# Performance work log

Hardware: AMD Instinct MI355X
Metric: run time of the kernel (lower is better)

Reference implementation:

```python
import jax, jax.numpy as jnp
import numpy as np

# ---- fixed opt values from source ----
B = 10
IN_C = 3
IN_HW = 64
OUT_VIEW_N = 8
OUT_H = 128
OUT_W = 128
RENDER_DEPTH = 1.0
LATENT = 512
KHOM2DTO3D = np.array([[64, 0, 0, 32], [0, -64, 0, 32], [0, 0, -1, 0], [0, 0, 0, 1]], dtype=np.float32)


def quat_to_rotmat(q):
    # q: [V,4] (w,x,y,z)
    w, x, y, z = q[:, 0], q[:, 1], q[:, 2], q[:, 3]
    R = jnp.stack([
        1 - 2 * (y * y + z * z), 2 * (x * y - w * z), 2 * (x * z + w * y),
        2 * (x * y + w * z), 1 - 2 * (x * x + z * z), 2 * (y * z - w * x),
        2 * (x * z - w * y), 2 * (y * z + w * x), 1 - 2 * (x * x + y * y),
    ], axis=-1).reshape(-1, 3, 3)
    return R


def conv(x, w, b, stride=2):
    y = jax.lax.conv_general_dilated(x, w, (stride, stride), 'SAME',
                                     dimension_numbers=('NCHW', 'OIHW', 'NCHW'))
    return y + b[None, :, None, None]


def deconv(x, w, b):
    # stride-2 transposed conv, kernel 4, SAME-like (doubles spatial size)
    y = jax.lax.conv_transpose(x, w, (2, 2), 'SAME',
                               dimension_numbers=('NCHW', 'OIHW', 'NCHW'),
                               transpose_kernel=True)
    return y + b[None, :, None, None]


def setup_inputs() -> dict:
    key = jax.random.key(0)
    ks = jax.random.split(key, 24)
    s = 0.05
    d = {}
    d['x'] = jax.random.normal(ks[0], (B, IN_C, IN_HW, IN_HW), dtype=jnp.float32)
    # encoder convs: 3->96->128->192->256 (stride 2 each, 64->4), then fc -> latent
    enc_ch = [IN_C, 96, 128, 192, 256]
    for i in range(4):
        d[f'ew{i}'] = jax.random.normal(ks[1 + i], (enc_ch[i + 1], enc_ch[i], 3, 3)) * s
        d[f'eb{i}'] = jnp.zeros((enc_ch[i + 1],), jnp.float32)
    d['efw'] = jax.random.normal(ks[5], (256 * 4 * 4, LATENT)) * s
    d['efb'] = jnp.zeros((LATENT,), jnp.float32)
    # decoder: fc latent -> 256*4*4, deconvs 256->192->128->96->64->48 (4->128)
    d['dfw'] = jax.random.normal(ks[6], (LATENT, 256 * 4 * 4)) * s
    d['dfb'] = jnp.zeros((256 * 4 * 4,), jnp.float32)
    dec_ch = [256, 192, 128, 96, 64, 48]
    for i in range(5):
        d[f'dw{i}'] = jax.random.normal(ks[7 + i], (dec_ch[i], dec_ch[i + 1], 4, 4)) * s
        d[f'db{i}'] = jnp.zeros((dec_ch[i + 1],), jnp.float32)
    # heads: 1x1 conv -> XYZ (V*3) and mask logits (V)
    d['xyzw'] = jax.random.normal(ks[12], (OUT_VIEW_N * 3, dec_ch[-1], 1, 1)) * s
    d['xyzb'] = jnp.zeros((OUT_VIEW_N * 3,), jnp.float32)
    d['maskw'] = jax.random.normal(ks[13], (OUT_VIEW_N, dec_ch[-1], 1, 1)) * s
    d['maskb'] = jnp.zeros((OUT_VIEW_N,), jnp.float32)
    # fuseTrans: fixed per-view quaternions (normalized)
    q = jax.random.normal(ks[14], (OUT_VIEW_N, 4))
    d['fuseTrans'] = q / jnp.linalg.norm(q, axis=-1, keepdims=True)
    return d


def _forward(x, ew0, eb0, ew1, eb1, ew2, eb2, ew3, eb3, efw, efb,
             dfw, dfb, dw0, db0, dw1, db1, dw2, db2, dw3, db3, dw4, db4,
             xyzw, xyzb, maskw, maskb, fuseTrans):
    relu = jax.nn.relu
    # encoder
    h = relu(conv(x, ew0, eb0))
    h = relu(conv(h, ew1, eb1))
    h = relu(conv(h, ew2, eb2))
    h = relu(conv(h, ew3, eb3))  # [B,256,4,4]
    latent = relu(h.reshape(B, -1) @ efw + efb)
    # decoder
    h = relu(latent @ dfw + dfb).reshape(B, 256, 4, 4)
    h = relu(deconv(h, dw0, db0))
    h = relu(deconv(h, dw1, db1))
    h = relu(deconv(h, dw2, db2))
    h = relu(deconv(h, dw3, db3))
    h = relu(deconv(h, dw4, db4))  # [B,48,128,128]
    XYZ = conv(h, xyzw, xyzb, stride=1)        # [B,V*3,H,W]
    maskLogit = conv(h, maskw, maskb, stride=1)  # [B,V,H,W]
    # ---- fuse3D ----
    V, H, W = OUT_VIEW_N, OUT_H, OUT_W
    XYZ = XYZ.reshape(B, V, 3, H, W)
    X = XYZ[:, :, 0].reshape(B, V, -1)
    Y = XYZ[:, :, 1].reshape(B, V, -1)
    Z = XYZ[:, :, 2].reshape(B, V, -1) + RENDER_DEPTH  # predicted depth offset
    ones = jnp.ones_like(X)
    XYZhom = jnp.stack([X, Y, Z, ones], axis=2)  # [B,V,4,HW]
    # inverse-project 2D grid coords + depth to 3D camera coords
    Kinv = jnp.asarray(np.linalg.inv(KHOM2DTO3D))  # [4,4]
    XYZcam = jnp.einsum('ij,bvjn->bvin', Kinv, XYZhom)[:, :, :3]  # [B,V,3,HW]
    # rotate each view into canonical frame via fuseTrans quaternions
    R = quat_to_rotmat(fuseTrans)  # [V,3,3] cam->world
    RT = jnp.swapaxes(R, 1, 2)
    XYZid = jnp.einsum('vij,bvjn->bvin', RT, XYZcam)  # [B,V,3,HW]
    XYZid = jnp.transpose(XYZid, (0, 2, 1, 3)).reshape(B, 3, V * H * W)
    ML = maskLogit.reshape(B, 1, V * H * W)
    return XYZid, ML


def reference(x, ew0, eb0, ew1, eb1, ew2, eb2, ew3, eb3, efw, efb,
              dfw, dfb, dw0, db0, dw1, db1, dw2, db2, dw3, db3, dw4, db4,
              xyzw, xyzb, maskw, maskb, fuseTrans):
    return _forward(x, ew0, eb0, ew1, eb1, ew2, eb2, ew3, eb3, efw, efb,
                    dfw, dfb, dw0, db0, dw1, db1, dw2, db2, dw3, db3, dw4, db4,
                    xyzw, xyzb, maskw, maskb, fuseTrans)
```

## Files before the change

### kernel.cpp

```cpp
#include <hip/hip_runtime.h>

#define CDIV(a,b) (((a)+(b)-1)/(b))

typedef short short8v __attribute__((ext_vector_type(8)));
typedef float f32x4 __attribute__((ext_vector_type(4)));

__device__ __forceinline__ ushort f2bf(float v) {
    uint u = __float_as_uint(v);
    return (ushort)((u + 0x7FFF + ((u >> 16) & 1)) >> 16);
}

__global__ __launch_bounds__(256) void conv3x3_c3(const float* __restrict__ in,
    const float* __restrict__ w, const float* __restrict__ bias, float* __restrict__ out)
{
    int idx = blockIdx.x * 256 + threadIdx.x;
    int ox = idx & 31; int t = idx >> 5;
    int oy = t & 31;   t >>= 5;
    int co = t % 96;   int b = t / 96;
    float acc = bias[co];
    const float* wp  = w + co * 27;
    const float* ipb = in + (size_t)b * 3 * 64 * 64;
    #pragma unroll
    for (int ci = 0; ci < 3; ++ci) {
        #pragma unroll
        for (int ky = 0; ky < 3; ++ky) {
            int iy = 2 * oy + ky;
            #pragma unroll
            for (int kx = 0; kx < 3; ++kx) {
                int ix = 2 * ox + kx;
                if (iy < 64 && ix < 64)
                    acc = fmaf(wp[ci * 9 + ky * 3 + kx], ipb[(ci * 64 + iy) * 64 + ix], acc);
            }
        }
    }
    out[idx] = fmaxf(acc, 0.f);
}

template<int CIN,int COUT,int HIN,int WIN,int SPLITS,int CK,int CO_R>
__global__ __launch_bounds__(256) void conv_splitk_big(const float* __restrict__ in,
    const float* __restrict__ w, float* __restrict__ partial)
{
    constexpr int HOUT = HIN/2, WOUT = WIN/2;
    constexpr int SP = HOUT * WOUT;
    static_assert(SP == 256, "one output px per thread");
    constexpr int HP = HIN + 1, WP = WIN + 2;
    constexpr int CSL = CIN / SPLITS;
    constexpr int NCH = CSL / CK;
    static_assert(CSL % CK == 0, "CK must divide ci slice");
    constexpr int SELEM = CK * HP * WP;
    constexpr int NLD = (SELEM + 255) / 256;
    __shared__ float sb[SELEM];

    const int b = blockIdx.y, s = blockIdx.z;
    const int co_base = blockIdx.x * CO_R;
    const int oy = threadIdx.x >> 4, ox = threadIdx.x & 15;
    const int ci00 = s * CSL;
    const float* inb = in + (size_t)b * CIN * HIN * WIN;

    float rg[NLD];
    auto load_chunk = [&](int ci0) {
        #pragma unroll
        for (int j = 0; j < NLD; ++j) {
            int i = threadIdx.x + j * 256;
            float v = 0.f;
            if (i < SELEM) {
                int c = i % WP; int r = (i / WP) % HP; int cl = i / (WP * HP);
                if (r < HIN && c < WIN) v = inb[((size_t)(ci0 + cl) * HIN + r) * WIN + c];
            }
            rg[j] = v;
        }
    };
    load_chunk(ci00);

    float acc[CO_R] = {};
    for (int ch = 0; ch < NCH; ++ch) {
        #pragma unroll
        for (int j = 0; j < NLD; ++j) {
            int i = threadIdx.x + j * 256;
            if (i < SELEM) sb[i] = rg[j];
        }
        __syncthreads();
        if (ch + 1 < NCH) load_chunk(ci00 + (ch + 1) * CK);

        #pragma unroll
        for (int cl = 0; cl < CK; ++cl) {
            const float* sp = &sb[(cl * HP + 2 * oy) * WP + 2 * ox];
            float x[3][3];
            #pragma unroll
            for (int dy = 0; dy < 3; ++dy) {
                float2 f = *(const float2*)&sp[dy * WP];
                x[dy][0] = f.x; x[dy][1] = f.y; x[dy][2] = sp[dy * WP + 2];
            }
            int ci = ci00 + ch * CK + cl;
            const float* wp = w + ((size_t)co_base * CIN + ci) * 9;
            #pragma unroll
            for (int r = 0; r < CO_R; ++r) {
                const float* wr = wp + (size_t)r * CIN * 9;
                #pragma unroll
                for (int dy = 0; dy < 3; ++dy)
                    #pragma unroll
                    for (int dx = 0; dx < 3; ++dx)
                        acc[r] = fmaf(wr[dy * 3 + dx], x[dy][dx], acc[r]);
            }
        }
        __syncthreads();
    }
    #pragma unroll
    for (int r = 0; r < CO_R; ++r)
        partial[(((size_t)s * 10 + b) * COUT + co_base + r) * SP + threadIdx.x] = acc[r];
}

template<int CIN,int COUT,int HIN,int WIN,int CK,int CO_R,int COS>
__global__ __launch_bounds__(256) void conv_small_splitk(const float* __restrict__ in,
    const float* __restrict__ w, float* __restrict__ partial)
{
    constexpr int HOUT = HIN/2, WOUT = WIN/2;
    constexpr int SP = HOUT * WOUT;
    static_assert(SP * COS == 256, "block covers SP x COS");
    constexpr int HP = HIN + 1, WP = WIN + 2;
    __shared__ float sb[CK * HP * WP];
    const int b = blockIdx.y;
    const int s = blockIdx.z;
    const int sp_i = threadIdx.x % SP;
    const int slot = threadIdx.x / SP;
    const int co_base = (blockIdx.x * COS + slot) * CO_R;
    const int oy = sp_i / WOUT, ox = sp_i % WOUT;
    const int ci0 = s * CK;
    const float* inb = in + (size_t)b * CIN * HIN * WIN;

    for (int i = threadIdx.x; i < CK * HP * WP; i += 256) {
        int c = i % WP; int r = (i / WP) % HP; int cl = i / (WP * HP);
        float v = 0.f;
        if (r < HIN && c < WIN) v = inb[((size_t)(ci0 + cl) * HIN + r) * WIN + c];
        sb[i] = v;
    }
    __syncthreads();

    float acc[CO_R] = {};
    #pragma unroll
    for (int cl = 0; cl < CK; ++cl) {
        const float* sp = &sb[(cl * HP + 2 * oy) * WP + 2 * ox];
        float x[3][3];
        #pragma unroll
        for (int dy = 0; dy < 3; ++dy) {
            float2 f = *(const float2*)&sp[dy * WP];
            x[dy][0] = f.x; x[dy][1] = f.y; x[dy][2] = sp[dy * WP + 2];
        }
        const float* wp = w + ((size_t)co_base * CIN + (ci0 + cl)) * 9;
        #pragma unroll
        for (int r = 0; r < CO_R; ++r) {
            const float* wr = wp + (size_t)r * CIN * 9;
            #pragma unroll
            for (int dy = 0; dy < 3; ++dy)
                #pragma unroll
                for (int dx = 0; dx < 3; ++dx)
                    acc[r] = fmaf(wr[dy * 3 + dx], x[dy][dx], acc[r]);
        }
    }
    #pragma unroll
    for (int r = 0; r < CO_R; ++r)
        partial[(((size_t)s * 10 + b) * COUT + co_base + r) * SP + sp_i] = acc[r];
}

template<int COUT,int SP,int S>
__global__ void conv_reduce_relu(const float* __restrict__ partial, const float* __restrict__ bias,
                                 float* __restrict__ out, int total)
{
    int i = blockIdx.x * 256 + threadIdx.x;
    if (i >= total) return;
    int sp = i % SP; int co = (i / SP) % COUT; int b = i / (SP * COUT);
    float acc = bias[co];
    #pragma unroll
    for (int s = 0; s < S; ++s) acc += partial[(((size_t)s * 10 + b) * COUT + co) * SP + sp];
    out[i] = fmaxf(acc, 0.f);
}

template<int CIN,int COUT>
__global__ __launch_bounds__(256) void prep_wA_g(const float* __restrict__ w, ushort* __restrict__ Abuf)
{
    constexpr int MFR = COUT / 16, NSL = CIN / 8;
    constexpr int TOTAL = 4 * MFR * NSL * 64 * 8;
    int idx = blockIdx.x * 256 + threadIdx.x;
    if (idx >= TOTAL) return;
    int e = idx & 7; int t2 = idx >> 3;
    int lane = t2 & 63; t2 >>= 6;
    int s = t2 % NSL; t2 /= NSL;
    int m = t2 % MFR; int q = t2 / MFR;
    int co = m * 16 + (lane & 15);
    int k = s * 32 + (lane >> 4) * 8 + e;
    int tap = k / CIN, ci = k % CIN;
    const int widx[4][4] = {{5,7,13,15},{4,6,12,14},{1,3,9,11},{0,2,8,10}};
    float v = w[((size_t)ci * COUT + co) * 16 + widx[q][tap]];
    Abuf[idx] = f2bf(v);
}

template<int CIN,int COUT,int HIN,int QPB,int MS>
__global__ __launch_bounds__(256) void deconv_mfma_g(const float* __restrict__ X,
    const ushort* __restrict__ Abuf, const float* __restrict__ bias, float* __restrict__ out)
{
    constexpr int MFR = COUT / 16, NSL = CIN / 8, STR = CIN + 8;
    constexpr int MPB = MFR / MS;
    constexpr int ZQ = 4 / QPB;
    constexpr int WOUT = 2 * HIN, PLANE = 4 * HIN * HIN;
    __shared__ __align__(16) ushort Xs[100 * STR];
    __shared__ float sbias[COUT];
    const int tid = threadIdx.x;
    constexpr int TW = HIN / 8;
    const int t0 = (blockIdx.x / TW) * 8, u0 = (blockIdx.x % TW) * 8;
    const int b = blockIdx.y;
    const int zq = blockIdx.z % ZQ;
    const int ms = blockIdx.z / ZQ;

    const float* Xb = X + (size_t)b * CIN * HIN * HIN;
    for (int i = tid; i < CIN * 100; i += 256) {
        int ci = i / 100, p = i % 100;
        int r = p / 10, c = p % 10;
        int gt = t0 - 1 + r, gu = u0 - 1 + c;
        float v = 0.f;
        if (gt >= 0 && gt < HIN && gu >= 0 && gu < HIN)
            v = Xb[((size_t)ci * HIN + gt) * HIN + gu];
        Xs[p * STR + ci] = f2bf(v);
    }
    if (tid < COUT) sbias[tid] = bias[tid];
    __syncthreads();

    const int w = tid >> 6, lane = tid & 63;
    const int ncol = lane & 15, kg = lane >> 4;
    const int r_n = 2 * w + (ncol >> 3), c_n = ncol & 7;

    #pragma unroll
    for (int qz = 0; qz < QPB; ++qz) {
        const int q = zq * QPB + qz;
        const int py = q >> 1, px = q & 1;
        int ptap[4];
        #pragma unroll
        for (int tp = 0; tp < 4; ++tp) {
            int dy = py - (tp >> 1);
            int dx = px - (tp & 1);
            ptap[tp] = ((r_n + 1 + dy) * 10 + (c_n + 1 + dx)) * STR;
        }
        #pragma unroll
        for (int mm = 0; mm < MPB; ++mm) {
            const int m = ms * MPB + mm;
            f32x4 acc = {0.f, 0.f, 0.f, 0.f};
            const ushort* ab = Abuf + (((size_t)(q * MFR + m) * NSL) * 64 + lane) * 8;
            #pragma unroll
            for (int s = 0; s < NSL; ++s) {
                short8v a = *(const short8v*)(ab + (size_t)s * 64 * 8);
                int tap = (s * 32) / CIN;
                int ci0 = (s * 32) % CIN + kg * 8;
                short8v bf = *(const short8v*)(&Xs[ptap[tap] + ci0]);
                acc = __builtin_amdgcn_mfma_f32_16x16x32_bf16(a, bf, acc, 0, 0, 0);
            }
            int t = t0 + r_n, u = u0 + c_n;
            size_t base = ((size_t)(b * COUT + m * 16 + kg * 4) * (2 * HIN) + (2 * t + py)) * WOUT + (2 * u + px);
            #pragma unroll
            for (int jj = 0; jj < 4; ++jj) {
                float v = acc[jj] + sbias[m * 16 + kg * 4 + jj];
                out[base + (size_t)jj * PLANE] = fmaxf(v, 0.f);
            }
        }
    }
}

__global__ __launch_bounds__(256) void deconv_mfma_d0(const float* __restrict__ X,
    const ushort* __restrict__ Abuf, const float* __restrict__ bias, float* __restrict__ out)
{
    constexpr int CIN = 256, COUT = 192, MFR = 12, NSL = 32, STR = CIN + 8;
    __shared__ __align__(16) ushort Xs[36 * STR];
    __shared__ float sbias[COUT];
    const int tid = threadIdx.x;
    const int b = blockIdx.y, q = blockIdx.z;

    const float* Xb = X + (size_t)b * CIN * 16;
    for (int i = tid; i < CIN * 36; i += 256) {
        int ci = i / 36, p = i % 36;
        int r = p / 6, c = p % 6;
        int gt = r - 1, gu = c - 1;
        float v = 0.f;
        if (gt >= 0 && gt < 4 && gu >= 0 && gu < 4)
            v = Xb[(ci * 4 + gt) * 4 + gu];
        Xs[p * STR + ci] = f2bf(v);
    }
    if (tid < COUT) sbias[tid] = bias[tid];
    __syncthreads();

    const int w = tid >> 6, lane = tid & 63;
    const int ncol = lane & 15, kg = lane >> 4;
    const int r_n = ncol >> 2, c_n = ncol & 3;
    const int py = q >> 1, px = q & 1;

    int ptap[4];
    #pragma unroll
    for (int tp = 0; tp < 4; ++tp) {
        int dy = py - (tp >> 1);
        int dx = px - (tp & 1);
        ptap[tp] = ((r_n + 1 + dy) * 6 + (c_n + 1 + dx)) * STR;
    }
    #pragma unroll
    for (int j = 0; j < 3; ++j) {
        const int m = w + 4 * j;
        f32x4 acc = {0.f, 0.f, 0.f, 0.f};
        const ushort* ab = Abuf + (((size_t)(q * MFR + m) * NSL) * 64 + lane) * 8;
        #pragma unroll
        for (int s = 0; s < NSL; ++s) {
            short8v a = *(const short8v*)(ab + (size_t)s * 64 * 8);
            int tap = s >> 3, ci0 = (s & 7) * 32 + kg * 8;
            short8v bf = *(const short8v*)(&Xs[ptap[tap] + ci0]);
            acc = __builtin_amdgcn_mfma_f32_16x16x32_bf16(a, bf, acc, 0, 0, 0);
        }
        size_t base = ((size_t)(b * COUT + m * 16 + kg * 4) * 8 + (2 * r_n + py)) * 8 + (2 * c_n + px);
        #pragma unroll
        for (int jj = 0; jj < 4; ++jj) {
            float v = acc[jj] + sbias[m * 16 + kg * 4 + jj];
            out[base + (size_t)jj * 64] = fmaxf(v, 0.f);
        }
    }
}

template<int KC>
__global__ __launch_bounds__(256) void fc_splitk(const float* __restrict__ in,
    const float* __restrict__ W, float* __restrict__ partial, int K, int N)
{
    __shared__ float s_in[10 * KC];
    const int o = blockIdx.x * 256 + threadIdx.x;
    const int k0 = blockIdx.y * KC;
    for (int i = threadIdx.x; i < 10 * KC; i += 256) {
        int b = i / KC, k = i % KC;
        s_in[i] = in[(size_t)b * K + k0 + k];
    }
    __syncthreads();

    float acc[10];
    #pragma unroll
    for (int b = 0; b < 10; ++b) acc[b] = 0.f;
    const float* wp = W + (size_t)k0 * N + o;
    #pragma unroll 4
    for (int k = 0; k < KC; ++k) {
        float wv = wp[(size_t)k * N];
        #pragma unroll
        for (int b = 0; b < 10; ++b) acc[b] = fmaf(wv, s_in[b * KC + k], acc[b]);
    }
    float* pp = partial + ((size_t)blockIdx.y * 10) * N + o;
    #pragma unroll
    for (int b = 0; b < 10; ++b) pp[(size_t)b * N] = acc[b];
}

__global__ void fc_reduce_relu(const float* __restrict__ partial, const float* __restrict__ bias,
                               float* __restrict__ out, int N, int S)
{
    int i = blockIdx.x * 256 + threadIdx.x;
    if (i >= 10 * N) return;
    int o = i % N, b = i / N;
    float acc = bias[o];
    for (int s = 0; s < S; ++s) acc += partial[((size_t)s * 10 + b) * N + o];
    out[(size_t)b * N + o] = fmaxf(acc, 0.f);
}

__global__ __launch_bounds__(256) void final_fused_v2(const float* __restrict__ h,
    const float* __restrict__ xyzw, const float* __restrict__ xyzb,
    const float* __restrict__ maskw, const float* __restrict__ maskb,
    const float* __restrict__ quat, float* __restrict__ out)
{
    const int V = 8, HW = 128 * 128, C = 48, Bn = 10, VHW = V * HW;
    __shared__ float4 sh[48 * 32];
    int b = blockIdx.y, tile = blockIdx.x;
    const float4* hb = (const float4*)h;
    for (int i = threadIdx.x; i < C * 32; i += 256) {
        int ci = i >> 5, p = i & 31;
        sh[i] = hb[(size_t)(b * C + ci) * (HW / 4) + tile * 32 + p];
    }
    __syncthreads();

    int pl = threadIdx.x & 31, v = threadIdx.x >> 5;
    float4 xr = {0,0,0,0}, yr = {0,0,0,0}, zr = {0,0,0,0}, mm = {0,0,0,0};
    const float* wx = xyzw + (size_t)(v * 3 + 0) * C;
    const float* wy = xyzw + (size_t)(v * 3 + 1) * C;
    const float* wz = xyzw + (size_t)(v * 3 + 2) * C;
    const float* wm = maskw + (size_t)v * C;
    for (int ci = 0; ci < C; ++ci) {
        float4 hv = sh[ci * 32 + pl];
        float a;
        a = wx[ci]; xr.x += a*hv.x; xr.y += a*hv.y; xr.z += a*hv.z; xr.w += a*hv.w;
        a = wy[ci]; yr.x += a*hv.x; yr.y += a*hv.y; yr.z += a*hv.z; yr.w += a*hv.w;
        a = wz[ci]; zr.x += a*hv.x; zr.y += a*hv.y; zr.z += a*hv.z; zr.w += a*hv.w;
        a = wm[ci]; mm.x += a*hv.x; mm.y += a*hv.y; mm.z += a*hv.z; mm.w += a*hv.w;
    }
    float bxv = xyzb[v * 3 + 0], byv = xyzb[v * 3 + 1], bzv = xyzb[v * 3 + 2], bmv = maskb[v];

    float qw = quat[v*4+0], qx = quat[v*4+1], qy = quat[v*4+2], qz = quat[v*4+3];
    float R00 = 1.f - 2.f*(qy*qy + qz*qz), R01 = 2.f*(qx*qy - qw*qz), R02 = 2.f*(qx*qz + qw*qy);
    float R10 = 2.f*(qx*qy + qw*qz), R11 = 1.f - 2.f*(qx*qx + qz*qz), R12 = 2.f*(qy*qz - qw*qx);
    float R20 = 2.f*(qx*qz - qw*qy), R21 = 2.f*(qy*qz + qw*qx), R22 = 1.f - 2.f*(qx*qx + qy*qy);

    float4 o0, o1, o2, om;
    float* X = (float*)&xr; float* Y = (float*)&yr; float* Z = (float*)&zr; float* M = (float*)&mm;
    float* O0 = (float*)&o0; float* O1 = (float*)&o1; float* O2 = (float*)&o2; float* OM = (float*)&om;
    #pragma unroll
    for (int j = 0; j < 4; ++j) {
        float camX = (X[j] + bxv) * (1.f / 64.f) - 0.5f;
        float camY = -(Y[j] + byv) * (1.f / 64.f) + 0.5f;
        float camZ = -((Z[j] + bzv) + 1.0f);
        O0[j] = R00 * camX + R10 * camY + R20 * camZ;
        O1[j] = R01 * camX + R11 * camY + R21 * camZ;
        O2[j] = R02 * camX + R12 * camY + R22 * camZ;
        OM[j] = M[j] + bmv;
    }

    size_t o = (size_t)v * HW + tile * 128 + pl * 4;
    float4* op = (float4*)out;
    op[((size_t)(b * 3 + 0) * VHW + o) >> 2] = o0;
    op[((size_t)(b * 3 + 1) * VHW + o) >> 2] = o1;
    op[((size_t)(b * 3 + 2) * VHW + o) >> 2] = o2;
    op[((size_t)Bn * 3 * VHW + (size_t)b * VHW + o) >> 2] = om;
}


extern "C" void kernel_launch(void* const* d_in, const int* in_sizes, int n_in,
                              void* d_out, int out_size, void* d_ws, size_t ws_size,
                              hipStream_t stream)
{
    const float* x    = (const float*)d_in[0];
    const float* ew0  = (const float*)d_in[1];
    const float* eb0  = (const float*)d_in[2];
    const float* ew1  = (const float*)d_in[3];
    const float* eb1  = (const float*)d_in[4];
    const float* ew2  = (const float*)d_in[5];
    const float* eb2  = (const float*)d_in[6];
    const float* ew3  = (const float*)d_in[7];
    const float* eb3  = (const float*)d_in[8];
    const float* efw  = (const float*)d_in[9];
    const float* efb  = (const float*)d_in[10];
    const float* dfw  = (const float*)d_in[11];
    const float* dfb  = (const float*)d_in[12];
    const float* dw0  = (const float*)d_in[13];
    const float* db0  = (const float*)d_in[14];
    const float* dw1  = (const float*)d_in[15];
    const float* db1  = (const float*)d_in[16];
    const float* dw2  = (const float*)d_in[17];
    const float* db2  = (const float*)d_in[18];
    const float* dw3  = (const float*)d_in[19];
    const float* db3  = (const float*)d_in[20];
    const float* dw4  = (const float*)d_in[21];
    const float* db4  = (const float*)d_in[22];
    const float* xyzw = (const float*)d_in[23];
    const float* xyzb = (const float*)d_in[24];
    const float* maskw= (const float*)d_in[25];
    const float* maskb= (const float*)d_in[26];
    const float* quat = (const float*)d_in[27];
    float* out = (float*)d_out;

    float* A   = (float*)d_ws;
    float* Bb  = A + 7864320;
    float* P1  = A;
    float* L   = A + 1120000;
    float* P2  = Bb + 1000000;
    float* H0  = Bb;
    float* PC1 = A + 2000000;
    float* PC2 = A + 2000000;
    float* PC3 = Bb + 500000;
    ushort* Abuf4 = (ushort*)(Bb + 2700000);
    ushort* Abuf3 = (ushort*)(A + 1000000);
    ushort* Abuf2 = (ushort*)(A + 1200000);
    ushort* Abuf1 = (ushort*)(A + 1400000);
    ushort* Abuf0 = (ushort*)(A + 1600000);

    const int TB = 256;

    prep_wA_g< 64, 48><<< 192, 256, 0, stream>>>(dw4, Abuf4);
    prep_wA_g< 96, 64><<< 384, 256, 0, stream>>>(dw3, Abuf3);
    prep_wA_g<128, 96><<< 768, 256, 0, stream>>>(dw2, Abuf2);
    prep_wA_g<192,128><<<1536, 256, 0, stream>>>(dw1, Abuf1);
    prep_wA_g<256,192><<<3072, 256, 0, stream>>>(dw0, Abuf0);

    conv3x3_c3<<<3840, 256, 0, stream>>>(x, ew0, eb0, A);
    conv_splitk_big<96,128,32,32,16,6,16><<<dim3(8,10,16), 256, 0, stream>>>(A, ew1, PC1);
    conv_reduce_relu<128,256,16><<<CDIV(327680,TB), TB, 0, stream>>>(PC1, eb1, Bb, 327680);
    conv_small_splitk<128,192,16,16,16,3,4><<<dim3(16,10,8), 256, 0, stream>>>(Bb, ew2, PC2);
    conv_reduce_relu<192,64,8><<<CDIV(122880,TB), TB, 0, stream>>>(PC2, eb2, A, 122880);
    conv_small_splitk<192,256,8,8,16,1,16><<<dim3(16,10,12), 256, 0, stream>>>(A, ew3, PC3);
    conv_reduce_relu<256,16,12><<<CDIV(40960,TB), TB, 0, stream>>>(PC3, eb3, Bb, 40960);

    fc_splitk<32><<<dim3(2, 128), 256, 0, stream>>>(Bb, efw, P1, 4096, 512);
    fc_reduce_relu<<<CDIV(10 * 512, TB), TB, 0, stream>>>(P1, efb, L, 512, 128);
    fc_splitk<32><<<dim3(16, 16), 256, 0, stream>>>(L, dfw, P2, 512, 4096);
    fc_reduce_relu<<<CDIV(10 * 4096, TB), TB, 0, stream>>>(P2, dfb, H0, 4096, 16);

    deconv_mfma_d0<<<dim3(1, 10, 4), 256, 0, stream>>>(H0, Abuf0, db0, A);
    deconv_mfma_g<192,128,  8, 1, 8><<<dim3( 1, 10, 32), 256, 0, stream>>>(A, Abuf1, db1, Bb);
    deconv_mfma_g<128, 96, 16, 1, 3><<<dim3( 4, 10, 12), 256, 0, stream>>>(Bb, Abuf2, db2, A);
    deconv_mfma_g< 96, 64, 32, 1, 1><<<dim3(16, 10,  4), 256, 0, stream>>>(A, Abuf3, db3, Bb);
    deconv_mfma_g< 64, 48, 64, 2, 1><<<dim3(64, 10,  2), 256, 0, stream>>>(Bb, Abuf4, db4, A);

    final_fused_v2<<<dim3(128, 10), 256, 0, stream>>>(A, xyzw, xyzb, maskw, maskb, quat, out);
}
```

Measured before the change: 320.9 us.

## Replace split-K FP32 encoder convs with bf16 MFMA implicit-GEMM kernels

```diff
diff --git a/kernel.cpp b/kernel.cpp
--- a/kernel.cpp
+++ b/kernel.cpp
@@ -36,143 +36,75 @@
     out[idx] = fmaxf(acc, 0.f);
 }
 
-template<int CIN,int COUT,int HIN,int WIN,int SPLITS,int CK,int CO_R>
-__global__ __launch_bounds__(256) void conv_splitk_big(const float* __restrict__ in,
-    const float* __restrict__ w, float* __restrict__ partial)
-{
-    constexpr int HOUT = HIN/2, WOUT = WIN/2;
-    constexpr int SP = HOUT * WOUT;
-    static_assert(SP == 256, "one output px per thread");
-    constexpr int HP = HIN + 1, WP = WIN + 2;
-    constexpr int CSL = CIN / SPLITS;
-    constexpr int NCH = CSL / CK;
-    static_assert(CSL % CK == 0, "CK must divide ci slice");
-    constexpr int SELEM = CK * HP * WP;
-    constexpr int NLD = (SELEM + 255) / 256;
-    __shared__ float sb[SELEM];
-
-    const int b = blockIdx.y, s = blockIdx.z;
-    const int co_base = blockIdx.x * CO_R;
-    const int oy = threadIdx.x >> 4, ox = threadIdx.x & 15;
-    const int ci00 = s * CSL;
-    const float* inb = in + (size_t)b * CIN * HIN * WIN;
-
-    float rg[NLD];
-    auto load_chunk = [&](int ci0) {
-        #pragma unroll
-        for (int j = 0; j < NLD; ++j) {
-            int i = threadIdx.x + j * 256;
-            float v = 0.f;
-            if (i < SELEM) {
-                int c = i % WP; int r = (i / WP) % HP; int cl = i / (WP * HP);
-                if (r < HIN && c < WIN) v = inb[((size_t)(ci0 + cl) * HIN + r) * WIN + c];
-            }
-            rg[j] = v;
-        }
-    };
-    load_chunk(ci00);
-
-    float acc[CO_R] = {};
-    for (int ch = 0; ch < NCH; ++ch) {
-        #pragma unroll
-        for (int j = 0; j < NLD; ++j) {
-            int i = threadIdx.x + j * 256;
-            if (i < SELEM) sb[i] = rg[j];
-        }
-        __syncthreads();
-        if (ch + 1 < NCH) load_chunk(ci00 + (ch + 1) * CK);
-
-        #pragma unroll
-        for (int cl = 0; cl < CK; ++cl) {
-            const float* sp = &sb[(cl * HP + 2 * oy) * WP + 2 * ox];
-            float x[3][3];
-            #pragma unroll
-            for (int dy = 0; dy < 3; ++dy) {
-                float2 f = *(const float2*)&sp[dy * WP];
-                x[dy][0] = f.x; x[dy][1] = f.y; x[dy][2] = sp[dy * WP + 2];
-            }
-            int ci = ci00 + ch * CK + cl;
-            const float* wp = w + ((size_t)co_base * CIN + ci) * 9;
-            #pragma unroll
-            for (int r = 0; r < CO_R; ++r) {
-                const float* wr = wp + (size_t)r * CIN * 9;
-                #pragma unroll
-                for (int dy = 0; dy < 3; ++dy)
-                    #pragma unroll
-                    for (int dx = 0; dx < 3; ++dx)
-                        acc[r] = fmaf(wr[dy * 3 + dx], x[dy][dx], acc[r]);
-            }
-        }
-        __syncthreads();
-    }
-    #pragma unroll
-    for (int r = 0; r < CO_R; ++r)
-        partial[(((size_t)s * 10 + b) * COUT + co_base + r) * SP + threadIdx.x] = acc[r];
-}
-
-template<int CIN,int COUT,int HIN,int WIN,int CK,int CO_R,int COS>
-__global__ __launch_bounds__(256) void conv_small_splitk(const float* __restrict__ in,
-    const float* __restrict__ w, float* __restrict__ partial)
-{
-    constexpr int HOUT = HIN/2, WOUT = WIN/2;
-    constexpr int SP = HOUT * WOUT;
-    static_assert(SP * COS == 256, "block covers SP x COS");
-    constexpr int HP = HIN + 1, WP = WIN + 2;
-    __shared__ float sb[CK * HP * WP];
-    const int b = blockIdx.y;
-    const int s = blockIdx.z;
-    const int sp_i = threadIdx.x % SP;
-    const int slot = threadIdx.x / SP;
-    const int co_base = (blockIdx.x * COS + slot) * CO_R;
-    const int oy = sp_i / WOUT, ox = sp_i % WOUT;
-    const int ci0 = s * CK;
-    const float* inb = in + (size_t)b * CIN * HIN * WIN;
-
-    for (int i = threadIdx.x; i < CK * HP * WP; i += 256) {
-        int c = i % WP; int r = (i / WP) % HP; int cl = i / (WP * HP);
+template<int CIN,int COUT>
+__global__ __launch_bounds__(256) void prep_wA_conv(const float* __restrict__ w, ushort* __restrict__ Abuf)
+{
+    constexpr int MFR = COUT / 16, NSL = 9 * CIN / 32;
+    constexpr int TOTAL = MFR * NSL * 64 * 8;
+    int idx = blockIdx.x * 256 + threadIdx.x;
+    if (idx >= TOTAL) return;
+    int e = idx & 7; int t2 = idx >> 3;
+    int lane = t2 & 63; t2 >>= 6;
+    int s = t2 % NSL; int m = t2 / NSL;
+    int co = m * 16 + (lane & 15);
+    int k = s * 32 + (lane >> 4) * 8 + e;
+    int tap = k / CIN, ci = k % CIN;
+    float v = w[((size_t)co * CIN + ci) * 9 + tap];
+    Abuf[idx] = f2bf(v);
+}
+
+template<int CIN,int COUT,int HOUT>
+__global__ __launch_bounds__(256) void conv_mfma_g(const float* __restrict__ X,
+    const ushort* __restrict__ Abuf, const float* __restrict__ bias, float* __restrict__ out)
+{
+    constexpr int HIN = 2 * HOUT;
+    constexpr int NSL = 9 * CIN / 32, STR = CIN + 8;
+    constexpr int TW = HOUT / 4;
+    __shared__ __align__(16) ushort Xs[81 * STR];
+    __shared__ float sbias[COUT];
+    const int tid = threadIdx.x;
+    const int oy0 = (blockIdx.x / TW) * 4, ox0 = (blockIdx.x % TW) * 4;
+    const int b = blockIdx.y, ms = blockIdx.z;
+
+    const float* Xb = X + (size_t)b * CIN * HIN * HIN;
+    for (int i = tid; i < CIN * 81; i += 256) {
+        int ci = i / 81, p = i % 81;
+        int r = p / 9, c = p % 9;
+        int gy = 2 * oy0 + r, gx = 2 * ox0 + c;
         float v = 0.f;
-        if (r < HIN && c < WIN) v = inb[((size_t)(ci0 + cl) * HIN + r) * WIN + c];
-        sb[i] = v;
-    }
+        if (gy < HIN && gx < HIN) v = Xb[((size_t)ci * HIN + gy) * HIN + gx];
+        Xs[p * STR + ci] = f2bf(v);
+    }
+    if (tid < COUT) sbias[tid] = bias[tid];
     __syncthreads();
 
-    float acc[CO_R] = {};
-    #pragma unroll
-    for (int cl = 0; cl < CK; ++cl) {
-        const float* sp = &sb[(cl * HP + 2 * oy) * WP + 2 * ox];
-        float x[3][3];
-        #pragma unroll
-        for (int dy = 0; dy < 3; ++dy) {
-            float2 f = *(const float2*)&sp[dy * WP];
-            x[dy][0] = f.x; x[dy][1] = f.y; x[dy][2] = sp[dy * WP + 2];
-        }
-        const float* wp = w + ((size_t)co_base * CIN + (ci0 + cl)) * 9;
-        #pragma unroll
-        for (int r = 0; r < CO_R; ++r) {
-            const float* wr = wp + (size_t)r * CIN * 9;
-            #pragma unroll
-            for (int dy = 0; dy < 3; ++dy)
-                #pragma unroll
-                for (int dx = 0; dx < 3; ++dx)
-                    acc[r] = fmaf(wr[dy * 3 + dx], x[dy][dx], acc[r]);
-        }
-    }
-    #pragma unroll
-    for (int r = 0; r < CO_R; ++r)
-        partial[(((size_t)s * 10 + b) * COUT + co_base + r) * SP + sp_i] = acc[r];
-}
-
-template<int COUT,int SP,int S>
-__global__ void conv_reduce_relu(const float* __restrict__ partial, const float* __restrict__ bias,
-                                 float* __restrict__ out, int total)
-{
-    int i = blockIdx.x * 256 + threadIdx.x;
-    if (i >= total) return;
-    int sp = i % SP; int co = (i / SP) % COUT; int b = i / (SP * COUT);
-    float acc = bias[co];
-    #pragma unroll
-    for (int s = 0; s < S; ++s) acc += partial[(((size_t)s * 10 + b) * COUT + co) * SP + sp];
-    out[i] = fmaxf(acc, 0.f);
+    const int w = tid >> 6, lane = tid & 63;
+    const int ncol = lane & 15, kg = lane >> 4;
+    const int r_n = ncol >> 2, c_n = ncol & 3;
+
+    int ptap[9];
+    #pragma unroll
+    for (int tp = 0; tp < 9; ++tp) {
+        int ky = tp / 3, kx = tp % 3;
+        ptap[tp] = ((2 * r_n + ky) * 9 + (2 * c_n + kx)) * STR;
+    }
+
+    const int m = ms * 4 + w;
+    f32x4 acc = {0.f, 0.f, 0.f, 0.f};
+    const ushort* ab = Abuf + ((size_t)m * NSL * 64 + lane) * 8;
+    #pragma unroll
+    for (int s = 0; s < NSL; ++s) {
+        short8v a = *(const short8v*)(ab + (size_t)s * 64 * 8);
+        int tap = (s * 32) / CIN;
+        int ci0 = (s * 32) % CIN + kg * 8;
+        short8v bf = *(const short8v*)(&Xs[ptap[tap] + ci0]);
+        acc = __builtin_amdgcn_mfma_f32_16x16x32_bf16(a, bf, acc, 0, 0, 0);
+    }
+    int oy = oy0 + r_n, ox = ox0 + c_n;
+    size_t base = ((size_t)(b * COUT + m * 16 + kg * 4) * HOUT + oy) * HOUT + ox;
+    #pragma unroll
+    for (int jj = 0; jj < 4; ++jj)
+        out[base + (size_t)jj * HOUT * HOUT] = fmaxf(acc[jj] + sbias[m * 16 + kg * 4 + jj], 0.f);
 }
 
 template<int CIN,int COUT>
@@ -456,14 +388,14 @@
     float* L   = A + 1120000;
     float* P2  = Bb + 1000000;
     float* H0  = Bb;
-    float* PC1 = A + 2000000;
-    float* PC2 = A + 2000000;
-    float* PC3 = Bb + 500000;
-    ushort* Abuf4 = (ushort*)(Bb + 2700000);
-    ushort* Abuf3 = (ushort*)(A + 1000000);
-    ushort* Abuf2 = (ushort*)(A + 1200000);
-    ushort* Abuf1 = (ushort*)(A + 1400000);
-    ushort* Abuf0 = (ushort*)(A + 1600000);
+    ushort* Abuf4  = (ushort*)(Bb + 2700000);
+    ushort* Abuf3  = (ushort*)(A + 1000000);
+    ushort* Abuf2  = (ushort*)(A + 1200000);
+    ushort* Abuf1  = (ushort*)(A + 1400000);
+    ushort* Abuf0  = (ushort*)(A + 1600000);
+    ushort* AbufC1 = (ushort*)(A + 2000000);
+    ushort* AbufC2 = (ushort*)(A + 2100000);
+    ushort* AbufC3 = (ushort*)(A + 2250000);
 
     const int TB = 256;
 
@@ -472,14 +404,14 @@
     prep_wA_g<128, 96><<< 768, 256, 0, stream>>>(dw2, Abuf2);
     prep_wA_g<192,128><<<1536, 256, 0, stream>>>(dw1, Abuf1);
     prep_wA_g<256,192><<<3072, 256, 0, stream>>>(dw0, Abuf0);
+    prep_wA_conv< 96,128><<< 432, 256, 0, stream>>>(ew1, AbufC1);
+    prep_wA_conv<128,192><<< 864, 256, 0, stream>>>(ew2, AbufC2);
+    prep_wA_conv<192,256><<<1728, 256, 0, stream>>>(ew3, AbufC3);
 
     conv3x3_c3<<<3840, 256, 0, stream>>>(x, ew0, eb0, A);
-    conv_splitk_big<96,128,32,32,16,6,16><<<dim3(8,10,16), 256, 0, stream>>>(A, ew1, PC1);
-    conv_reduce_relu<128,256,16><<<CDIV(327680,TB), TB, 0, stream>>>(PC1, eb1, Bb, 327680);
-    conv_small_splitk<128,192,16,16,16,3,4><<<dim3(16,10,8), 256, 0, stream>>>(Bb, ew2, PC2);
-    conv_reduce_relu<192,64,8><<<CDIV(122880,TB), TB, 0, stream>>>(PC2, eb2, A, 122880);
-    conv_small_splitk<192,256,8,8,16,1,16><<<dim3(16,10,12), 256, 0, stream>>>(A, ew3, PC3);
-    conv_reduce_relu<256,16,12><<<CDIV(40960,TB), TB, 0, stream>>>(PC3, eb3, Bb, 40960);
+    conv_mfma_g< 96,128,16><<<dim3(16, 10, 2), 256, 0, stream>>>(A,  AbufC1, eb1, Bb);
+    conv_mfma_g<128,192, 8><<<dim3( 4, 10, 3), 256, 0, stream>>>(Bb, AbufC2, eb2, A);
+    conv_mfma_g<192,256, 4><<<dim3( 1, 10, 4), 256, 0, stream>>>(A,  AbufC3, eb3, Bb);
 
     fc_splitk<32><<<dim3(2, 128), 256, 0, stream>>>(Bb, efw, P1, 4096, 512);
     fc_reduce_relu<<<CDIV(10 * 512, TB), TB, 0, stream>>>(P1, efb, L, 512, 128);
```

New measurement: 320.5 us. About the same (-0.1%).
